# Kernel tuning notes

Hardware: AMD Instinct MI355X
Metric: run time of the kernel (lower is better)

Reference implementation:

```python
import jax, jax.numpy as jnp
import numpy as np

N = 50000        # nodes
E = 800000       # edges (before self loops)
F_IN = 64        # num_features
DIM = 64         # num_hidden
C = 10           # num_classes
G = 256          # graphs in batch
NEG_SLOPE = 0.2


def setup_inputs() -> dict:
    key = jax.random.key(0)
    ks = jax.random.split(key, 20)
    def w(k, shape, fan_in):
        return jax.random.normal(k, shape, dtype=jnp.float32) / np.sqrt(fan_in)
    x = jax.random.normal(ks[0], (N, F_IN), dtype=jnp.float32)
    edge_index = jax.random.randint(ks[1], (2, E), 0, N, dtype=jnp.int64)
    batch = jnp.sort(jax.random.randint(ks[2], (N,), 0, G, dtype=jnp.int64))
    return {
        "x": x, "edge_index": edge_index, "batch": batch,
        "w1": w(ks[3], (F_IN, DIM), F_IN), "as1": w(ks[4], (DIM,), DIM), "ad1": w(ks[5], (DIM,), DIM), "b1": jnp.zeros((DIM,), jnp.float32),
        "w2": w(ks[6], (DIM, DIM), DIM),  "as2": w(ks[7], (DIM,), DIM), "ad2": w(ks[8], (DIM,), DIM), "b2": jnp.zeros((DIM,), jnp.float32),
        "w3": w(ks[9], (DIM, DIM), DIM),  "as3": w(ks[10], (DIM,), DIM), "ad3": w(ks[11], (DIM,), DIM), "b3": jnp.zeros((DIM,), jnp.float32),
        "fc1_w": w(ks[12], (DIM, DIM), DIM), "fc1_b": jnp.zeros((DIM,), jnp.float32),
        "fc2_w": w(ks[13], (DIM, C), DIM),   "fc2_b": jnp.zeros((C,), jnp.float32),
    }


def _gat_conv(x, src, dst, w, a_src, a_dst, b, n_nodes):
    # PyG GATConv, heads=1: h = x W; e_ij = LeakyReLU(a_src.h_j + a_dst.h_i);
    # alpha = segment-softmax over edges grouped by target i; out_i = sum_j alpha_ij h_j + b
    h = x @ w                                   # [N, DIM]
    alpha_s = h @ a_src                         # [N]
    alpha_d = h @ a_dst                         # [N]
    e = jax.nn.leaky_relu(alpha_s[src] + alpha_d[dst], NEG_SLOPE)  # [E']
    e_max = jax.ops.segment_max(e, dst, num_segments=n_nodes)
    e_exp = jnp.exp(e - e_max[dst])
    denom = jax.ops.segment_sum(e_exp, dst, num_segments=n_nodes)
    alpha = e_exp / (denom[dst] + 1e-16)        # [E']
    out = jax.ops.segment_sum(alpha[:, None] * h[src], dst, num_segments=n_nodes)
    return out + b


def _l2_normalize(x):
    nrm = jnp.linalg.norm(x, axis=1, keepdims=True)
    return x / jnp.maximum(nrm, 1e-12)


def reference(x, edge_index, batch, w1, as1, ad1, b1, w2, as2, ad2, b2,
              w3, as3, ad3, b3, fc1_w, fc1_b, fc2_w, fc2_b):
    n = x.shape[0]
    loops = jnp.arange(n, dtype=edge_index.dtype)
    src = jnp.concatenate([edge_index[0], loops])   # add_self_loops=True (PyG default)
    dst = jnp.concatenate([edge_index[1], loops])
    h = _gat_conv(x, src, dst, w1, as1, ad1, b1, n)
    h = jax.nn.relu(_l2_normalize(h))
    h = _gat_conv(h, src, dst, w2, as2, ad2, b2, n)
    h = jax.nn.relu(_l2_normalize(h))
    h = _gat_conv(h, src, dst, w3, as3, ad3, b3, n)
    h = jax.nn.relu(_l2_normalize(h))
    g = jax.ops.segment_sum(h, batch, num_segments=G)   # global_add_pool -> [G, DIM]
    g = jax.nn.relu(g @ fc1_w + fc1_b)
    logits = g @ fc2_w + fc2_b
    return jax.nn.log_softmax(logits, axis=-1)
```

## Files before the change

### kernel.cpp

```cpp
#include <hip/hip_runtime.h>
#include <hip/hip_bf16.h>
#include <math.h>

#define DIM 64
#define GNUM 256
#define CNUM 10

__device__ __forceinline__ unsigned bfpack(float a, float b) {
    unsigned ua = __builtin_bit_cast(unsigned, a);
    unsigned ub = __builtin_bit_cast(unsigned, b);
    ua += 0x7fffu + ((ua >> 16) & 1u);
    ub += 0x7fffu + ((ub >> 16) & 1u);
    return (ua >> 16) | (ub & 0xffff0000u);
}
__device__ __forceinline__ float bflo(unsigned u) { return __builtin_bit_cast(float, u << 16); }
__device__ __forceinline__ float bfhi(unsigned u) { return __builtin_bit_cast(float, u & 0xffff0000u); }
__device__ __forceinline__ float bfs(unsigned short u) { return __builtin_bit_cast(float, (unsigned)u << 16); }

__global__ void deg_rank_kernel(const int* __restrict__ ei, int E, int N,
                                int* __restrict__ deg, int* __restrict__ rank) {
    int i = blockIdx.x * blockDim.x + threadIdx.x;
    int EP = E + N;
    if (i >= EP) return;
    int d = (i < E) ? ei[E + i] : (i - E);
    rank[i] = atomicAdd(&deg[d], 1);
}

__global__ __launch_bounds__(256) void scan_misc(const int* __restrict__ deg, int* __restrict__ part, int n, int nb,
                                                 const int* __restrict__ batch, int N,
                                                 int* __restrict__ gstart) {
    int bid = blockIdx.x;
    if (bid < nb) {
        __shared__ int ws[4];
        int i = bid * 256 + threadIdx.x;
        int v = (i < n) ? deg[i] : 0;
        #pragma unroll
        for (int d = 32; d >= 1; d >>= 1) v += __shfl_xor(v, d);
        if ((threadIdx.x & 63) == 0) ws[threadIdx.x >> 6] = v;
        __syncthreads();
        if (threadIdx.x == 0) part[bid] = ws[0] + ws[1] + ws[2] + ws[3];
    } else {
        for (int g = threadIdx.x; g <= GNUM; g += 256) {
            int lo = 0, hi = N;
            while (lo < hi) { int mid = (lo + hi) >> 1; if (batch[mid] < g) lo = mid + 1; else hi = mid; }
            gstart[g] = lo;
        }
    }
}

__global__ __launch_bounds__(256) void scan_down(const int* __restrict__ deg, const int* __restrict__ part,
                                                 int* __restrict__ offs, int n) {
    __shared__ int ws[4];
    __shared__ int base_s;
    int tid = threadIdx.x, lane = tid & 63, wid = tid >> 6;
    int pv = (tid < (int)blockIdx.x) ? part[tid] : 0;
    #pragma unroll
    for (int d = 32; d >= 1; d >>= 1) pv += __shfl_xor(pv, d);
    if (lane == 0) ws[wid] = pv;
    __syncthreads();
    if (tid == 0) base_s = ws[0] + ws[1] + ws[2] + ws[3];
    __syncthreads();
    int i = blockIdx.x * 256 + tid;
    int v = (i < n) ? deg[i] : 0;
    int x = v;
    #pragma unroll
    for (int d = 1; d < 64; d <<= 1) { int t = __shfl_up(x, d); if (lane >= d) x += t; }
    if (lane == 63) ws[wid] = x;
    __syncthreads();
    int add = base_s;
    for (int w = 0; w < wid; ++w) add += ws[w];
    if (i < n) offs[i] = add + x - v;
    if (i == n - 1) offs[n] = add + x;
}

#define XSTR 68
template<bool BF16IN>
__device__ __forceinline__ void mm_tile_body(int bid,
                                             const void* __restrict__ in_, const float* __restrict__ W,
                                             const float* __restrict__ a_s, const float* __restrict__ a_d,
                                             unsigned* __restrict__ hb, float* __restrict__ as_,
                                             float* __restrict__ ad_, int N) {
    __shared__ float Ws[DIM * DIM];
    __shared__ float xT[XSTR * DIM];
    int tid = threadIdx.x;
    int base = bid * 64;

    const float4* W4 = (const float4*)W;
    float4* Ws4 = (float4*)Ws;
    #pragma unroll
    for (int i = 0; i < 4; ++i) Ws4[tid + 256 * i] = W4[tid + 256 * i];

    {
        int row = tid >> 2;
        int kb = (tid & 3) << 4;
        int grow = base + row;
        int crow = grow < N ? grow : N - 1;
        if (BF16IN) {
            const unsigned* xr = (const unsigned*)in_ + ((size_t)crow << 5) + (kb >> 1);
            uint4 u0 = *(const uint4*)xr;
            uint4 u1 = *(const uint4*)(xr + 4);
            xT[(kb + 0) * XSTR + row] = bflo(u0.x);  xT[(kb + 1) * XSTR + row] = bfhi(u0.x);
            xT[(kb + 2) * XSTR + row] = bflo(u0.y);  xT[(kb + 3) * XSTR + row] = bfhi(u0.y);
            xT[(kb + 4) * XSTR + row] = bflo(u0.z);  xT[(kb + 5) * XSTR + row] = bfhi(u0.z);
            xT[(kb + 6) * XSTR + row] = bflo(u0.w);  xT[(kb + 7) * XSTR + row] = bfhi(u0.w);
            xT[(kb + 8) * XSTR + row] = bflo(u1.x);  xT[(kb + 9) * XSTR + row] = bfhi(u1.x);
            xT[(kb + 10) * XSTR + row] = bflo(u1.y); xT[(kb + 11) * XSTR + row] = bfhi(u1.y);
            xT[(kb + 12) * XSTR + row] = bflo(u1.z); xT[(kb + 13) * XSTR + row] = bfhi(u1.z);
            xT[(kb + 14) * XSTR + row] = bflo(u1.w); xT[(kb + 15) * XSTR + row] = bfhi(u1.w);
        } else {
            const float4* xr = (const float4*)((const float*)in_ + ((size_t)crow << 6) + kb);
            float4 v0 = xr[0], v1 = xr[1], v2 = xr[2], v3 = xr[3];
            xT[(kb + 0) * XSTR + row] = v0.x;  xT[(kb + 1) * XSTR + row] = v0.y;
            xT[(kb + 2) * XSTR + row] = v0.z;  xT[(kb + 3) * XSTR + row] = v0.w;
            xT[(kb + 4) * XSTR + row] = v1.x;  xT[(kb + 5) * XSTR + row] = v1.y;
            xT[(kb + 6) * XSTR + row] = v1.z;  xT[(kb + 7) * XSTR + row] = v1.w;
            xT[(kb + 8) * XSTR + row] = v2.x;  xT[(kb + 9) * XSTR + row] = v2.y;
            xT[(kb + 10) * XSTR + row] = v2.z; xT[(kb + 11) * XSTR + row] = v2.w;
            xT[(kb + 12) * XSTR + row] = v3.x; xT[(kb + 13) * XSTR + row] = v3.y;
            xT[(kb + 14) * XSTR + row] = v3.z; xT[(kb + 15) * XSTR + row] = v3.w;
        }
    }
    __syncthreads();

    int tx = tid & 15, ty = tid >> 4;
    int c0 = tx << 2, r0 = ty << 2;
    float acc[4][4] = {{0.f}};
    #pragma unroll 8
    for (int k = 0; k < DIM; ++k) {
        float4 xv = *(const float4*)(xT + k * XSTR + r0);
        float4 wv = *(const float4*)(Ws + k * DIM + c0);
        acc[0][0] += xv.x * wv.x; acc[0][1] += xv.x * wv.y; acc[0][2] += xv.x * wv.z; acc[0][3] += xv.x * wv.w;
        acc[1][0] += xv.y * wv.x; acc[1][1] += xv.y * wv.y; acc[1][2] += xv.y * wv.z; acc[1][3] += xv.y * wv.w;
        acc[2][0] += xv.z * wv.x; acc[2][1] += xv.z * wv.y; acc[2][2] += xv.z * wv.z; acc[2][3] += xv.z * wv.w;
        acc[3][0] += xv.w * wv.x; acc[3][1] += xv.w * wv.y; acc[3][2] += xv.w * wv.z; acc[3][3] += xv.w * wv.w;
    }

    float4 av = *(const float4*)(a_s + c0);
    float4 dv = *(const float4*)(a_d + c0);
    #pragma unroll
    for (int ri = 0; ri < 4; ++ri) {
        int grow = base + r0 + ri;
        float s1 = acc[ri][0] * av.x + acc[ri][1] * av.y + acc[ri][2] * av.z + acc[ri][3] * av.w;
        float s2 = acc[ri][0] * dv.x + acc[ri][1] * dv.y + acc[ri][2] * dv.z + acc[ri][3] * dv.w;
        #pragma unroll
        for (int d = 1; d <= 8; d <<= 1) { s1 += __shfl_xor(s1, d); s2 += __shfl_xor(s2, d); }
        if (grow < N) {
            uint2 o;
            o.x = bfpack(acc[ri][0], acc[ri][1]);
            o.y = bfpack(acc[ri][2], acc[ri][3]);
            *(uint2*)(hb + ((size_t)grow << 5) + (tx << 1)) = o;
            if (tx == 0) { as_[grow] = s1; ad_[grow] = s2; }
        }
    }
}

__global__ __launch_bounds__(256) void mm_tile_bf(const unsigned* __restrict__ in, const float* __restrict__ W,
                                                  const float* __restrict__ a_s, const float* __restrict__ a_d,
                                                  unsigned* __restrict__ hb, float* __restrict__ as_,
                                                  float* __restrict__ ad_, int N) {
    mm_tile_body<true>(blockIdx.x, in, W, a_s, a_d, hb, as_, ad_, N);
}

__global__ __launch_bounds__(256) void mm_fill(const float* __restrict__ in, const float* __restrict__ W,
                                               const float* __restrict__ a_s, const float* __restrict__ a_d,
                                               unsigned* __restrict__ hb, float* __restrict__ as_,
                                               float* __restrict__ ad_, int N, int nbt,
                                               const int* __restrict__ ei, const int* __restrict__ rank, int E,
                                               const int* __restrict__ offs, int2* __restrict__ csr_sd) {
    int bid = blockIdx.x;
    if (bid < nbt) {
        mm_tile_body<false>(bid, in, W, a_s, a_d, hb, as_, ad_, N);
    } else {
        int i = (bid - nbt) * 256 + threadIdx.x;
        int EP = E + N;
        if (i >= EP) return;
        int s, d;
        if (i < E) { s = ei[i]; d = ei[E + i]; } else { s = i - E; d = i - E; }
        csr_sd[offs[d] + rank[i]] = make_int2(s, d);
    }
}

#define AGG_NPB 32
#define AGG_CAP 2048
__global__ __launch_bounds__(256) void gat_agg(const unsigned* __restrict__ hb,
                                               const int2* __restrict__ csr_sd,
                                               const float* __restrict__ as_,
                                               const float* __restrict__ ad_,
                                               const int* __restrict__ offs,
                                               const float* __restrict__ bias,
                                               unsigned* __restrict__ outb, int N) {
    __shared__ int soffs[AGG_NPB + 1];
    __shared__ float adl[AGG_NPB];
    __shared__ int2 lsw[AGG_CAP + 4];
    int tid = threadIdx.x;
    int base = blockIdx.x * AGG_NPB;
    if (tid <= AGG_NPB) {
        int n = base + tid;
        soffs[tid] = offs[n < N ? n : N];
    }
    if (tid < AGG_NPB) {
        int n = base + tid;
        adl[tid] = (n < N) ? ad_[n] : 0.f;
    }
    __syncthreads();
    int estart = soffs[0];
    int nE = soffs[AGG_NPB] - estart;
    bool inLds = (nE <= AGG_CAP);
    if (inLds) {
        for (int i = tid; i < nE; i += 256) {
            int2 sd = csr_sd[estart + i];
            float e = as_[sd.x] + adl[sd.y - base];
            e = (e > 0.f) ? e : 0.2f * e;
            lsw[i] = make_int2(sd.x, __builtin_bit_cast(int, expf(e)));
        }
        if (tid < 4) lsw[nE + tid] = make_int2(0, 0);
    }
    __syncthreads();

    int lane = tid & 63, wid = tid >> 6;
    int sub = lane >> 3, fg = lane & 7;
    int li = (wid << 3) + sub;
    int node = base + li;
    int ls = soffs[li] - estart;
    int deg = soffs[li + 1] - soffs[li];

    float a0 = 0.f, a1 = 0.f, a2 = 0.f, a3 = 0.f;
    float a4 = 0.f, a5 = 0.f, a6 = 0.f, a7 = 0.f, sw = 0.f;
    if (inLds) {
        for (int eb = 0; eb < deg; eb += 4) {
            int t = ls + eb;
            int2 eA = lsw[t], eB = lsw[t + 1], eC = lsw[t + 2], eD = lsw[t + 3];
            float wA = __builtin_bit_cast(float, eA.y);
            float wB = (eb + 1 < deg) ? __builtin_bit_cast(float, eB.y) : 0.f;
            float wC = (eb + 2 < deg) ? __builtin_bit_cast(float, eC.y) : 0.f;
            float wD = (eb + 3 < deg) ? __builtin_bit_cast(float, eD.y) : 0.f;
            const uint4 hA = *(const uint4*)(hb + ((size_t)eA.x << 5) + (fg << 2));
            const uint4 hB = *(const uint4*)(hb + ((size_t)eB.x << 5) + (fg << 2));
            const uint4 hC = *(const uint4*)(hb + ((size_t)eC.x << 5) + (fg << 2));
            const uint4 hD = *(const uint4*)(hb + ((size_t)eD.x << 5) + (fg << 2));
            sw += wA + wB + wC + wD;
            a0 += wA * bflo(hA.x) + wB * bflo(hB.x) + wC * bflo(hC.x) + wD * bflo(hD.x);
            a1 += wA * bfhi(hA.x) + wB * bfhi(hB.x) + wC * bfhi(hC.x) + wD * bfhi(hD.x);
            a2 += wA * bflo(hA.y) + wB * bflo(hB.y) + wC * bflo(hC.y) + wD * bflo(hD.y);
            a3 += wA * bfhi(hA.y) + wB * bfhi(hB.y) + wC * bfhi(hC.y) + wD * bfhi(hD.y);
            a4 += wA * bflo(hA.z) + wB * bflo(hB.z) + wC * bflo(hC.z) + wD * bflo(hD.z);
            a5 += wA * bfhi(hA.z) + wB * bfhi(hB.z) + wC * bfhi(hC.z) + wD * bfhi(hD.z);
            a6 += wA * bflo(hA.w) + wB * bflo(hB.w) + wC * bflo(hC.w) + wD * bflo(hD.w);
            a7 += wA * bfhi(hA.w) + wB * bfhi(hB.w) + wC * bfhi(hC.w) + wD * bfhi(hD.w);
        }
    } else {
        float adi = (node < N) ? ad_[node] : 0.f;
        for (int eb = 0; eb < deg; eb += 4) {
            int t = estart + ls + eb;
            float wv[4]; int sv[4];
            #pragma unroll
            for (int k = 0; k < 4; ++k) {
                int tt = t + k;
                int2 sd = (eb + k < deg) ? csr_sd[tt] : make_int2(0, 0);
                int s = sd.x; s = s < 0 ? 0 : (s >= N ? N - 1 : s);
                float e = as_[s] + adi;
                e = (e > 0.f) ? e : 0.2f * e;
                wv[k] = (eb + k < deg) ? expf(e) : 0.f;
                sv[k] = s;
            }
            #pragma unroll
            for (int k = 0; k < 4; ++k) {
                const uint4 hv = *(const uint4*)(hb + ((size_t)sv[k] << 5) + (fg << 2));
                sw += wv[k];
                a0 += wv[k] * bflo(hv.x); a1 += wv[k] * bfhi(hv.x);
                a2 += wv[k] * bflo(hv.y); a3 += wv[k] * bfhi(hv.y);
                a4 += wv[k] * bflo(hv.z); a5 += wv[k] * bfhi(hv.z);
                a6 += wv[k] * bflo(hv.w); a7 += wv[k] * bfhi(hv.w);
            }
        }
    }

    float inv = 1.f / (sw + 1e-16f);
    const float4 b0 = *(const float4*)(bias + (fg << 3));
    const float4 b1 = *(const float4*)(bias + (fg << 3) + 4);
    float o0 = a0 * inv + b0.x, o1 = a1 * inv + b0.y, o2 = a2 * inv + b0.z, o3 = a3 * inv + b0.w;
    float o4 = a4 * inv + b1.x, o5 = a5 * inv + b1.y, o6 = a6 * inv + b1.z, o7 = a7 * inv + b1.w;
    float n2 = o0 * o0 + o1 * o1 + o2 * o2 + o3 * o3 + o4 * o4 + o5 * o5 + o6 * o6 + o7 * o7;
    #pragma unroll
    for (int d = 1; d <= 4; d <<= 1) n2 += __shfl_xor(n2, d);
    float innrm = 1.f / fmaxf(sqrtf(n2), 1e-12f);
    if (node < N) {
        uint4 o;
        o.x = bfpack(fmaxf(o0 * innrm, 0.f), fmaxf(o1 * innrm, 0.f));
        o.y = bfpack(fmaxf(o2 * innrm, 0.f), fmaxf(o3 * innrm, 0.f));
        o.z = bfpack(fmaxf(o4 * innrm, 0.f), fmaxf(o5 * innrm, 0.f));
        o.w = bfpack(fmaxf(o6 * innrm, 0.f), fmaxf(o7 * innrm, 0.f));
        *(uint4*)(outb + ((size_t)node << 5) + (fg << 2)) = o;
    }
}

__global__ __launch_bounds__(256) void pool_mlp(const unsigned short* __restrict__ hb, const int* __restrict__ gstart,
                                                const float* __restrict__ fc1w, const float* __restrict__ fc1b,
                                                const float* __restrict__ fc2w, const float* __restrict__ fc2b,
                                                float* __restrict__ out) {
    __shared__ float W1[DIM * DIM];
    __shared__ float red[4 * DIM];
    __shared__ float tbuf[DIM];
    __shared__ float obuf[CNUM];
    int tid = threadIdx.x, lane = tid & 63, wv = tid >> 6;
    int gid = blockIdx.x;

    const float4* W4 = (const float4*)fc1w;
    float4* W1s = (float4*)W1;
    #pragma unroll
    for (int i = 0; i < 4; ++i) W1s[tid + 256 * i] = W4[tid + 256 * i];

    int s = gstart[gid], e = gstart[gid + 1];
    float acc = 0.f;
    for (int i = s + wv; i < e; i += 4) acc += bfs(hb[((size_t)i << 6) + lane]);
    red[wv * DIM + lane] = acc;
    __syncthreads();

    if (wv == 0) {
        float g = red[lane] + red[DIM + lane] + red[2 * DIM + lane] + red[3 * DIM + lane];
        float t = fc1b[lane];
        #pragma unroll
        for (int k = 0; k < DIM; ++k) t += __shfl(g, k) * W1[k * DIM + lane];
        t = fmaxf(t, 0.f);
        tbuf[lane] = t;
        float o = 0.f;
        if (lane < CNUM) {
            o = fc2b[lane];
            #pragma unroll
            for (int k = 0; k < DIM; ++k) o += tbuf[k] * fc2w[k * CNUM + lane];
            obuf[lane] = o;
        }
        if (lane < CNUM) {
            float mx = obuf[0];
            #pragma unroll
            for (int k = 1; k < CNUM; ++k) mx = fmaxf(mx, obuf[k]);
            float ssum = 0.f;
            #pragma unroll
            for (int k = 0; k < CNUM; ++k) ssum += expf(obuf[k] - mx);
            out[gid * CNUM + lane] = o - mx - logf(ssum);
        }
    }
}

static inline size_t align256(size_t x) { return (x + 255) & ~size_t(255); }

extern "C" void kernel_launch(void* const* d_in, const int* in_sizes, int n_in,
                              void* d_out, int out_size, void* d_ws, size_t ws_size,
                              hipStream_t stream) {
    const float* x     = (const float*)d_in[0];
    const int*   ei    = (const int*)d_in[1];
    const int*   batch = (const int*)d_in[2];
    const float* w1  = (const float*)d_in[3];
    const float* as1 = (const float*)d_in[4];
    const float* ad1 = (const float*)d_in[5];
    const float* b1  = (const float*)d_in[6];
    const float* w2  = (const float*)d_in[7];
    const float* as2 = (const float*)d_in[8];
    const float* ad2 = (const float*)d_in[9];
    const float* b2  = (const float*)d_in[10];
    const float* w3  = (const float*)d_in[11];
    const float* as3 = (const float*)d_in[12];
    const float* ad3 = (const float*)d_in[13];
    const float* b3  = (const float*)d_in[14];
    const float* fc1w = (const float*)d_in[15];
    const float* fc1b = (const float*)d_in[16];
    const float* fc2w = (const float*)d_in[17];
    const float* fc2b = (const float*)d_in[18];
    float* out = (float*)d_out;

    int N  = in_sizes[0] / DIM;
    int E  = in_sizes[1] / 2;
    int EP = E + N;
    int nb = (N + 255) / 256;

    char* p = (char*)d_ws;
    unsigned* hbf = (unsigned*)p; p += align256(sizeof(unsigned) * (size_t)N * (DIM / 2));
    unsigned* oAb = (unsigned*)p; p += align256(sizeof(unsigned) * (size_t)N * (DIM / 2));
    unsigned* oBb = (unsigned*)p; p += align256(sizeof(unsigned) * (size_t)N * (DIM / 2));
    float* as_  = (float*)p; p += align256(sizeof(float) * (size_t)N);
    float* ad_  = (float*)p; p += align256(sizeof(float) * (size_t)N);
    int*   deg  = (int*)p;   p += align256(sizeof(int) * (size_t)N);
    int*   offs = (int*)p;   p += align256(sizeof(int) * (size_t)(N + 1));
    int*   rank = (int*)p;   p += align256(sizeof(int) * (size_t)EP);
    int2*  csr_sd = (int2*)p; p += align256(sizeof(int2) * (size_t)EP);
    int*   part = (int*)p;   p += align256(sizeof(int) * (size_t)nb);
    int*   gst  = (int*)p;   p += align256(sizeof(int) * (size_t)(GNUM + 1));

    int nblk = (N + AGG_NPB - 1) / AGG_NPB;
    int nbt = (N + 63) / 64;
    int epBlocks = (EP + 255) / 256;

    hipMemsetAsync(deg, 0, sizeof(int) * (size_t)N, stream);
    deg_rank_kernel<<<epBlocks, 256, 0, stream>>>(ei, E, N, deg, rank);
    scan_misc<<<nb + 1, 256, 0, stream>>>(deg, part, N, nb, batch, N, gst);
    scan_down<<<nb, 256, 0, stream>>>(deg, part, offs, N);

    mm_fill<<<nbt + epBlocks, 256, 0, stream>>>(x, w1, as1, ad1, hbf, as_, ad_, N, nbt,
                                                ei, rank, E, offs, csr_sd);
    gat_agg<<<nblk, 256, 0, stream>>>(hbf, csr_sd, as_, ad_, offs, b1, oAb, N);
    mm_tile_bf<<<nbt, 256, 0, stream>>>(oAb, w2, as2, ad2, hbf, as_, ad_, N);
    gat_agg<<<nblk, 256, 0, stream>>>(hbf, csr_sd, as_, ad_, offs, b2, oBb, N);
    mm_tile_bf<<<nbt, 256, 0, stream>>>(oBb, w3, as3, ad3, hbf, as_, ad_, N);
    gat_agg<<<nblk, 256, 0, stream>>>(hbf, csr_sd, as_, ad_, offs, b3, oAb, N);

    pool_mlp<<<GNUM, 256, 0, stream>>>((const unsigned short*)oAb, gst, fc1w, fc1b, fc2w, fc2b, out);
}
```

Baseline: 266.5 us.

## Fuse GAT aggregation with next layer's linear transform in one kernel

Adds an agg_mm kernel that, per block of 64 nodes, computes the edge softmax weights into shared memory, aggregates neighbour features, applies bias, L2 normalisation and ReLU, then multiplies by the next layer's weight matrix and emits the next attention scalars. This removes the bf16 round-trip of intermediate activations through global memory and two kernel launches. Ping-pong buffers are added for h and the attention vectors. In exchange the block is smaller (64 nodes) with large shared memory use, which may lower occupancy and load balance relative to the separate aggregation kernel.

```diff
diff --git a/kernel.cpp b/kernel.cpp
--- a/kernel.cpp
+++ b/kernel.cpp
@@ -74,12 +74,11 @@
 }
 
 #define XSTR 68
-template<bool BF16IN>
-__device__ __forceinline__ void mm_tile_body(int bid,
-                                             const void* __restrict__ in_, const float* __restrict__ W,
-                                             const float* __restrict__ a_s, const float* __restrict__ a_d,
-                                             unsigned* __restrict__ hb, float* __restrict__ as_,
-                                             float* __restrict__ ad_, int N) {
+__device__ __forceinline__ void mm_tile_body_f32(int bid,
+                                                 const float* __restrict__ in_, const float* __restrict__ W,
+                                                 const float* __restrict__ a_s, const float* __restrict__ a_d,
+                                                 unsigned* __restrict__ hb, float* __restrict__ as_,
+                                                 float* __restrict__ ad_, int N) {
     __shared__ float Ws[DIM * DIM];
     __shared__ float xT[XSTR * DIM];
     int tid = threadIdx.x;
@@ -95,30 +94,16 @@
         int kb = (tid & 3) << 4;
         int grow = base + row;
         int crow = grow < N ? grow : N - 1;
-        if (BF16IN) {
-            const unsigned* xr = (const unsigned*)in_ + ((size_t)crow << 5) + (kb >> 1);
-            uint4 u0 = *(const uint4*)xr;
-            uint4 u1 = *(const uint4*)(xr + 4);
-            xT[(kb + 0) * XSTR + row] = bflo(u0.x);  xT[(kb + 1) * XSTR + row] = bfhi(u0.x);
-            xT[(kb + 2) * XSTR + row] = bflo(u0.y);  xT[(kb + 3) * XSTR + row] = bfhi(u0.y);
-            xT[(kb + 4) * XSTR + row] = bflo(u0.z);  xT[(kb + 5) * XSTR + row] = bfhi(u0.z);
-            xT[(kb + 6) * XSTR + row] = bflo(u0.w);  xT[(kb + 7) * XSTR + row] = bfhi(u0.w);
-            xT[(kb + 8) * XSTR + row] = bflo(u1.x);  xT[(kb + 9) * XSTR + row] = bfhi(u1.x);
-            xT[(kb + 10) * XSTR + row] = bflo(u1.y); xT[(kb + 11) * XSTR + row] = bfhi(u1.y);
-            xT[(kb + 12) * XSTR + row] = bflo(u1.z); xT[(kb + 13) * XSTR + row] = bfhi(u1.z);
-            xT[(kb + 14) * XSTR + row] = bflo(u1.w); xT[(kb + 15) * XSTR + row] = bfhi(u1.w);
-        } else {
-            const float4* xr = (const float4*)((const float*)in_ + ((size_t)crow << 6) + kb);
-            float4 v0 = xr[0], v1 = xr[1], v2 = xr[2], v3 = xr[3];
-            xT[(kb + 0) * XSTR + row] = v0.x;  xT[(kb + 1) * XSTR + row] = v0.y;
-            xT[(kb + 2) * XSTR + row] = v0.z;  xT[(kb + 3) * XSTR + row] = v0.w;
-            xT[(kb + 4) * XSTR + row] = v1.x;  xT[(kb + 5) * XSTR + row] = v1.y;
-            xT[(kb + 6) * XSTR + row] = v1.z;  xT[(kb + 7) * XSTR + row] = v1.w;
-            xT[(kb + 8) * XSTR + row] = v2.x;  xT[(kb + 9) * XSTR + row] = v2.y;
-            xT[(kb + 10) * XSTR + row] = v2.z; xT[(kb + 11) * XSTR + row] = v2.w;
-            xT[(kb + 12) * XSTR + row] = v3.x; xT[(kb + 13) * XSTR + row] = v3.y;
-            xT[(kb + 14) * XSTR + row] = v3.z; xT[(kb + 15) * XSTR + row] = v3.w;
-        }
+        const float4* xr = (const float4*)(in_ + ((size_t)crow << 6) + kb);
+        float4 v0 = xr[0], v1 = xr[1], v2 = xr[2], v3 = xr[3];
+        xT[(kb + 0) * XSTR + row] = v0.x;  xT[(kb + 1) * XSTR + row] = v0.y;
+        xT[(kb + 2) * XSTR + row] = v0.z;  xT[(kb + 3) * XSTR + row] = v0.w;
+        xT[(kb + 4) * XSTR + row] = v1.x;  xT[(kb + 5) * XSTR + row] = v1.y;
+        xT[(kb + 6) * XSTR + row] = v1.z;  xT[(kb + 7) * XSTR + row] = v1.w;
+        xT[(kb + 8) * XSTR + row] = v2.x;  xT[(kb + 9) * XSTR + row] = v2.y;
+        xT[(kb + 10) * XSTR + row] = v2.z; xT[(kb + 11) * XSTR + row] = v2.w;
+        xT[(kb + 12) * XSTR + row] = v3.x; xT[(kb + 13) * XSTR + row] = v3.y;
+        xT[(kb + 14) * XSTR + row] = v3.z; xT[(kb + 15) * XSTR + row] = v3.w;
     }
     __syncthreads();
 
@@ -154,13 +139,6 @@
     }
 }
 
-__global__ __launch_bounds__(256) void mm_tile_bf(const unsigned* __restrict__ in, const float* __restrict__ W,
-                                                  const float* __restrict__ a_s, const float* __restrict__ a_d,
-                                                  unsigned* __restrict__ hb, float* __restrict__ as_,
-                                                  float* __restrict__ ad_, int N) {
-    mm_tile_body<true>(blockIdx.x, in, W, a_s, a_d, hb, as_, ad_, N);
-}
-
 __global__ __launch_bounds__(256) void mm_fill(const float* __restrict__ in, const float* __restrict__ W,
                                                const float* __restrict__ a_s, const float* __restrict__ a_d,
                                                unsigned* __restrict__ hb, float* __restrict__ as_,
@@ -169,7 +147,7 @@
                                                const int* __restrict__ offs, int2* __restrict__ csr_sd) {
     int bid = blockIdx.x;
     if (bid < nbt) {
-        mm_tile_body<false>(bid, in, W, a_s, a_d, hb, as_, ad_, N);
+        mm_tile_body_f32(bid, in, W, a_s, a_d, hb, as_, ad_, N);
     } else {
         int i = (bid - nbt) * 256 + threadIdx.x;
         int EP = E + N;
@@ -177,6 +155,171 @@
         int s, d;
         if (i < E) { s = ei[i]; d = ei[E + i]; } else { s = i - E; d = i - E; }
         csr_sd[offs[d] + rank[i]] = make_int2(s, d);
+    }
+}
+
+#define FUS_NPB 64
+#define FUS_CAP 2560
+__global__ __launch_bounds__(256) void agg_mm(const unsigned* __restrict__ hbp,
+                                              const int2* __restrict__ csr_sd,
+                                              const float* __restrict__ asp,
+                                              const float* __restrict__ adp,
+                                              const int* __restrict__ offs,
+                                              const float* __restrict__ bias,
+                                              const float* __restrict__ W,
+                                              const float* __restrict__ a_s,
+                                              const float* __restrict__ a_d,
+                                              unsigned* __restrict__ hbn,
+                                              float* __restrict__ asn,
+                                              float* __restrict__ adn, int N) {
+    __shared__ int soffs[FUS_NPB + 1];
+    __shared__ float adl[FUS_NPB];
+    __shared__ int2 lsw[FUS_CAP + 4];
+    __shared__ float xT[XSTR * DIM];
+    float* Ws = (float*)lsw;
+
+    int tid = threadIdx.x;
+    int base = blockIdx.x * FUS_NPB;
+    if (tid <= FUS_NPB) {
+        int n = base + tid;
+        soffs[tid] = offs[n < N ? n : N];
+    }
+    if (tid < FUS_NPB) {
+        int n = base + tid;
+        adl[tid] = (n < N) ? adp[n] : 0.f;
+    }
+    __syncthreads();
+    int estart = soffs[0];
+    int nE = soffs[FUS_NPB] - estart;
+    bool inLds = (nE <= FUS_CAP);
+    if (inLds) {
+        for (int i = tid; i < nE; i += 256) {
+            int2 sd = csr_sd[estart + i];
+            float e = asp[sd.x] + adl[sd.y - base];
+            e = (e > 0.f) ? e : 0.2f * e;
+            lsw[i] = make_int2(sd.x, __builtin_bit_cast(int, expf(e)));
+        }
+        if (tid < 4) lsw[nE + tid] = make_int2(0, 0);
+    }
+    __syncthreads();
+
+    int lane = tid & 63, wid = tid >> 6;
+    int sub = lane >> 3, fg = lane & 7;
+
+    #pragma unroll
+    for (int p = 0; p < 2; ++p) {
+        int li = p * 32 + (wid << 3) + sub;
+        int node = base + li;
+        int ls = soffs[li] - estart;
+        int deg = soffs[li + 1] - soffs[li];
+
+        float a0 = 0.f, a1 = 0.f, a2 = 0.f, a3 = 0.f;
+        float a4 = 0.f, a5 = 0.f, a6 = 0.f, a7 = 0.f, sw = 0.f;
+        if (inLds) {
+            for (int eb = 0; eb < deg; eb += 4) {
+                int t = ls + eb;
+                int2 eA = lsw[t], eB = lsw[t + 1], eC = lsw[t + 2], eD = lsw[t + 3];
+                float wA = __builtin_bit_cast(float, eA.y);
+                float wB = (eb + 1 < deg) ? __builtin_bit_cast(float, eB.y) : 0.f;
+                float wC = (eb + 2 < deg) ? __builtin_bit_cast(float, eC.y) : 0.f;
+                float wD = (eb + 3 < deg) ? __builtin_bit_cast(float, eD.y) : 0.f;
+                const uint4 hA = *(const uint4*)(hbp + ((size_t)eA.x << 5) + (fg << 2));
+                const uint4 hB = *(const uint4*)(hbp + ((size_t)eB.x << 5) + (fg << 2));
+                const uint4 hC = *(const uint4*)(hbp + ((size_t)eC.x << 5) + (fg << 2));
+                const uint4 hD = *(const uint4*)(hbp + ((size_t)eD.x << 5) + (fg << 2));
+                sw += wA + wB + wC + wD;
+                a0 += wA * bflo(hA.x) + wB * bflo(hB.x) + wC * bflo(hC.x) + wD * bflo(hD.x);
+                a1 += wA * bfhi(hA.x) + wB * bfhi(hB.x) + wC * bfhi(hC.x) + wD * bfhi(hD.x);
+                a2 += wA * bflo(hA.y) + wB * bflo(hB.y) + wC * bflo(hC.y) + wD * bflo(hD.y);
+                a3 += wA * bfhi(hA.y) + wB * bfhi(hB.y) + wC * bfhi(hC.y) + wD * bfhi(hD.y);
+                a4 += wA * bflo(hA.z) + wB * bflo(hB.z) + wC * bflo(hC.z) + wD * bflo(hD.z);
+                a5 += wA * bfhi(hA.z) + wB * bfhi(hB.z) + wC * bfhi(hC.z) + wD * bfhi(hD.z);
+                a6 += wA * bflo(hA.w) + wB * bflo(hB.w) + wC * bflo(hC.w) + wD * bflo(hD.w);
+                a7 += wA * bfhi(hA.w) + wB * bfhi(hB.w) + wC * bfhi(hC.w) + wD * bfhi(hD.w);
+            }
+        } else {
+            float adi = adl[li];
+            for (int eb = 0; eb < deg; eb += 4) {
+                int t = estart + ls + eb;
+                float wv[4]; int sv[4];
+                #pragma unroll
+                for (int k = 0; k < 4; ++k) {
+                    int2 sd = (eb + k < deg) ? csr_sd[t + k] : make_int2(0, 0);
+                    int s = sd.x; s = s < 0 ? 0 : (s >= N ? N - 1 : s);
+                    float e = asp[s] + adi;
+                    e = (e > 0.f) ? e : 0.2f * e;
+                    wv[k] = (eb + k < deg) ? expf(e) : 0.f;
+                    sv[k] = s;
+                }
+                #pragma unroll
+                for (int k = 0; k < 4; ++k) {
+                    const uint4 hv = *(const uint4*)(hbp + ((size_t)sv[k] << 5) + (fg << 2));
+                    sw += wv[k];
+                    a0 += wv[k] * bflo(hv.x); a1 += wv[k] * bfhi(hv.x);
+                    a2 += wv[k] * bflo(hv.y); a3 += wv[k] * bfhi(hv.y);
+                    a4 += wv[k] * bflo(hv.z); a5 += wv[k] * bfhi(hv.z);
+                    a6 += wv[k] * bflo(hv.w); a7 += wv[k] * bfhi(hv.w);
+                }
+            }
+        }
+
+        float inv = 1.f / (sw + 1e-16f);
+        const float4 b0 = *(const float4*)(bias + (fg << 3));
+        const float4 b1 = *(const float4*)(bias + (fg << 3) + 4);
+        float o0 = a0 * inv + b0.x, o1 = a1 * inv + b0.y, o2 = a2 * inv + b0.z, o3 = a3 * inv + b0.w;
+        float o4 = a4 * inv + b1.x, o5 = a5 * inv + b1.y, o6 = a6 * inv + b1.z, o7 = a7 * inv + b1.w;
+        float n2 = o0 * o0 + o1 * o1 + o2 * o2 + o3 * o3 + o4 * o4 + o5 * o5 + o6 * o6 + o7 * o7;
+        #pragma unroll
+        for (int d = 1; d <= 4; d <<= 1) n2 += __shfl_xor(n2, d);
+        float innrm = 1.f / fmaxf(sqrtf(n2), 1e-12f);
+        if (node >= N) innrm = 0.f;
+        int kb = fg << 3;
+        xT[(kb + 0) * XSTR + li] = fmaxf(o0 * innrm, 0.f);
+        xT[(kb + 1) * XSTR + li] = fmaxf(o1 * innrm, 0.f);
+        xT[(kb + 2) * XSTR + li] = fmaxf(o2 * innrm, 0.f);
+        xT[(kb + 3) * XSTR + li] = fmaxf(o3 * innrm, 0.f);
+        xT[(kb + 4) * XSTR + li] = fmaxf(o4 * innrm, 0.f);
+        xT[(kb + 5) * XSTR + li] = fmaxf(o5 * innrm, 0.f);
+        xT[(kb + 6) * XSTR + li] = fmaxf(o6 * innrm, 0.f);
+        xT[(kb + 7) * XSTR + li] = fmaxf(o7 * innrm, 0.f);
+    }
+    __syncthreads();
+
+    const float4* W4 = (const float4*)W;
+    float4* Ws4 = (float4*)Ws;
+    #pragma unroll
+    for (int i = 0; i < 4; ++i) Ws4[tid + 256 * i] = W4[tid + 256 * i];
+    __syncthreads();
+
+    int tx = tid & 15, ty = tid >> 4;
+    int c0 = tx << 2, r0 = ty << 2;
+    float acc[4][4] = {{0.f}};
+    #pragma unroll 8
+    for (int k = 0; k < DIM; ++k) {
+        float4 xv = *(const float4*)(xT + k * XSTR + r0);
+        float4 wv = *(const float4*)(Ws + k * DIM + c0);
+        acc[0][0] += xv.x * wv.x; acc[0][1] += xv.x * wv.y; acc[0][2] += xv.x * wv.z; acc[0][3] += xv.x * wv.w;
+        acc[1][0] += xv.y * wv.x; acc[1][1] += xv.y * wv.y; acc[1][2] += xv.y * wv.z; acc[1][3] += xv.y * wv.w;
+        acc[2][0] += xv.z * wv.x; acc[2][1] += xv.z * wv.y; acc[2][2] += xv.z * wv.z; acc[2][3] += xv.z * wv.w;
+        acc[3][0] += xv.w * wv.x; acc[3][1] += xv.w * wv.y; acc[3][2] += xv.w * wv.z; acc[3][3] += xv.w * wv.w;
+    }
+
+    float4 av = *(const float4*)(a_s + c0);
+    float4 dv = *(const float4*)(a_d + c0);
+    #pragma unroll
+    for (int ri = 0; ri < 4; ++ri) {
+        int grow = base + r0 + ri;
+        float s1 = acc[ri][0] * av.x + acc[ri][1] * av.y + acc[ri][2] * av.z + acc[ri][3] * av.w;
+        float s2 = acc[ri][0] * dv.x + acc[ri][1] * dv.y + acc[ri][2] * dv.z + acc[ri][3] * dv.w;
+        #pragma unroll
+        for (int d = 1; d <= 8; d <<= 1) { s1 += __shfl_xor(s1, d); s2 += __shfl_xor(s2, d); }
+        if (grow < N) {
+            uint2 o;
+            o.x = bfpack(acc[ri][0], acc[ri][1]);
+            o.y = bfpack(acc[ri][2], acc[ri][3]);
+            *(uint2*)(hbn + ((size_t)grow << 5) + (tx << 1)) = o;
+            if (tx == 0) { asn[grow] = s1; adn[grow] = s2; }
+        }
     }
 }
 
@@ -255,8 +398,7 @@
             float wv[4]; int sv[4];
             #pragma unroll
             for (int k = 0; k < 4; ++k) {
-                int tt = t + k;
-                int2 sd = (eb + k < deg) ? csr_sd[tt] : make_int2(0, 0);
+                int2 sd = (eb + k < deg) ? csr_sd[t + k] : make_int2(0, 0);
                 int s = sd.x; s = s < 0 ? 0 : (s >= N ? N - 1 : s);
                 float e = as_[s] + adi;
                 e = (e > 0.f) ? e : 0.2f * e;
@@ -374,11 +516,13 @@
     int nb = (N + 255) / 256;
 
     char* p = (char*)d_ws;
-    unsigned* hbf = (unsigned*)p; p += align256(sizeof(unsigned) * (size_t)N * (DIM / 2));
+    unsigned* hbA = (unsigned*)p; p += align256(sizeof(unsigned) * (size_t)N * (DIM / 2));
+    unsigned* hbB = (unsigned*)p; p += align256(sizeof(unsigned) * (size_t)N * (DIM / 2));
     unsigned* oAb = (unsigned*)p; p += align256(sizeof(unsigned) * (size_t)N * (DIM / 2));
-    unsigned* oBb = (unsigned*)p; p += align256(sizeof(unsigned) * (size_t)N * (DIM / 2));
-    float* as_  = (float*)p; p += align256(sizeof(float) * (size_t)N);
-    float* ad_  = (float*)p; p += align256(sizeof(float) * (size_t)N);
+    float* asA  = (float*)p; p += align256(sizeof(float) * (size_t)N);
+    float* adA  = (float*)p; p += align256(sizeof(float) * (size_t)N);
+    float* asB  = (float*)p; p += align256(sizeof(float) * (size_t)N);
+    float* adB  = (float*)p; p += align256(sizeof(float) * (size_t)N);
     int*   deg  = (int*)p;   p += align256(sizeof(int) * (size_t)N);
     int*   offs = (int*)p;   p += align256(sizeof(int) * (size_t)(N + 1));
     int*   rank = (int*)p;   p += align256(sizeof(int) * (size_t)EP);
@@ -386,6 +530,7 @@
     int*   part = (int*)p;   p += align256(sizeof(int) * (size_t)nb);
     int*   gst  = (int*)p;   p += align256(sizeof(int) * (size_t)(GNUM + 1));
 
+    int nfb  = (N + FUS_NPB - 1) / FUS_NPB;
     int nblk = (N + AGG_NPB - 1) / AGG_NPB;
     int nbt = (N + 63) / 64;
     int epBlocks = (EP + 255) / 256;
@@ -395,13 +540,13 @@
     scan_misc<<<nb + 1, 256, 0, stream>>>(deg, part, N, nb, batch, N, gst);
     scan_down<<<nb, 256, 0, stream>>>(deg, part, offs, N);
 
-    mm_fill<<<nbt + epBlocks, 256, 0, stream>>>(x, w1, as1, ad1, hbf, as_, ad_, N, nbt,
+    mm_fill<<<nbt + epBlocks, 256, 0, stream>>>(x, w1, as1, ad1, hbA, asA, adA, N, nbt,
                                                 ei, rank, E, offs, csr_sd);
-    gat_agg<<<nblk, 256, 0, stream>>>(hbf, csr_sd, as_, ad_, offs, b1, oAb, N);
-    mm_tile_bf<<<nbt, 256, 0, stream>>>(oAb, w2, as2, ad2, hbf, as_, ad_, N);
-    gat_agg<<<nblk, 256, 0, stream>>>(hbf, csr_sd, as_, ad_, offs, b2, oBb, N);
-    mm_tile_bf<<<nbt, 256, 0, stream>>>(oBb, w3, as3, ad3, hbf, as_, ad_, N);
-    gat_agg<<<nblk, 256, 0, stream>>>(hbf, csr_sd, as_, ad_, offs, b3, oAb, N);
+    agg_mm<<<nfb, 256, 0, stream>>>(hbA, csr_sd, asA, adA, offs, b1, w2, as2, ad2,
+                                    hbB, asB, adB, N);
+    agg_mm<<<nfb, 256, 0, stream>>>(hbB, csr_sd, asB, adB, offs, b2, w3, as3, ad3,
+                                    hbA, asA, adA, N);
+    gat_agg<<<nblk, 256, 0, stream>>>(hbA, csr_sd, asA, adA, offs, b3, oAb, N);
 
     pool_mlp<<<GNUM, 256, 0, stream>>>((const unsigned short*)oAb, gst, fc1w, fc1b, fc2w, fc2b, out);
 }
```

Result: faster. 250.5 us (-6.0%).
